# Optimization experiments

Hardware: AMD Instinct MI355X
Metric: run time of the kernel (lower is better)

The kernel has to match this reference:

```python
import jax, jax.numpy as jnp
import numpy as np

B, N, D = 2, 2048, 512
H, DH = 8, 64
P = 64  # position_max_embedding


def setup_inputs() -> dict:
    key = jax.random.key(0)
    ks = jax.random.split(key, 8)
    s = 0.02
    return {
        "x": jax.random.normal(ks[0], (B, N, D), jnp.float32),
        "Wq": jax.random.normal(ks[1], (D, H * DH), jnp.float32) * s,
        "Wk": jax.random.normal(ks[2], (D, H * DH), jnp.float32) * s,
        "Wv": jax.random.normal(ks[3], (D, H * DH), jnp.float32) * s,
        "rel_pos": jax.random.normal(ks[4], (2 * P + 1, H), jnp.float32) * s,
        "c_emb": jax.random.uniform(ks[5], (2 * P + 1, H), jnp.float32, 0.5, 1.5),
        "Wo": jax.random.normal(ks[6], (H * DH, D), jnp.float32) * s,
        "bo": jnp.zeros((D,), jnp.float32),
    }


def reference(x, Wq, Wk, Wv, rel_pos, c_emb, Wo, bo):
    b, n, _ = x.shape
    scale = DH ** -0.5
    q = (x @ Wq).reshape(b, n, H, DH)
    k = (x @ Wk).reshape(b, n, H, DH)
    v = (x @ Wv).reshape(b, n, H, DH)
    # relative position index: j - i, clamped to [-P, P], shifted to [0, 2P]
    idx = jnp.clip(jnp.arange(n)[None, :] - jnp.arange(n)[:, None], -P, P) + P  # [n, n]
    pos_bias = rel_pos[idx]          # [n, n, H]
    c_gate = c_emb[idx]              # [n, n, H]
    sim = jnp.einsum('bihd,bjhd->bhij', q, k)  # [b, H, n, n]
    sim = (sim + pos_bias.transpose(2, 0, 1)[None]) * scale
    attn = jax.nn.softmax(sim, axis=-1) * c_gate.transpose(2, 0, 1)[None]
    out = jnp.einsum('bhij,bjhd->bihd', attn, v).reshape(b, n, H * DH)
    return out @ Wo + bo
```

## Files before the change

kernel.cpp:

```cpp
#include <hip/hip_runtime.h>
#include <stdint.h>

#define BB 2
#define NN 2048
#define DD 512
#define HH 8
#define DHH 64

typedef __attribute__((ext_vector_type(8))) short bf16x8;
typedef __attribute__((ext_vector_type(4))) float f32x4;

#define LOG2E 1.44269504088896340736f

#if __has_builtin(__builtin_amdgcn_exp2f)
#define QSCALE (0.125f * LOG2E)
#define EXP2(x) __builtin_amdgcn_exp2f(x)
#else
#define QSCALE 0.125f
#define EXP2(x) __expf(x)
#endif

static __device__ __forceinline__ unsigned short f2bf(float f) {
    union { float f; unsigned u; } v; v.f = f;
    unsigned r = v.u + 0x7fffu + ((v.u >> 16) & 1u);
    return (unsigned short)(r >> 16);
}

static __device__ __forceinline__ unsigned pkbf(float a, float b) {
    union { float f; unsigned u; } ua, ub; ua.f = a; ub.f = b;
    return ((ub.u + 0x8000u) & 0xffff0000u) | ((ua.u + 0x8000u) >> 16);
}

static __device__ __forceinline__ bf16x8 ld8(const unsigned short* p) {
    bf16x8 v; __builtin_memcpy(&v, p, 16); return v;
}

static __device__ __forceinline__ void gld_lds16(const void* g, void* l) {
    __builtin_amdgcn_global_load_lds((const __attribute__((address_space(1))) void*)g,
                                     (__attribute__((address_space(3))) void*)l, 16, 0, 0);
}

__global__ void ca_prep(const float* __restrict__ x,
                        const float* __restrict__ w0, const float* __restrict__ w1,
                        const float* __restrict__ w2, const float* __restrict__ w3,
                        unsigned short* __restrict__ xb, unsigned short* __restrict__ wts) {
    __shared__ float T[64][65];
    int bx = blockIdx.x;
    if (bx < 2048) {
        int gid = bx * 256 + threadIdx.x;
        float4 v = ((const float4*)x)[gid];
        ushort4 o;
        o.x = f2bf(v.x); o.y = f2bf(v.y); o.z = f2bf(v.z); o.w = f2bf(v.w);
        ((ushort4*)xb)[gid] = o;
        return;
    }
    int bb = bx - 2048;
    int z = bb >> 6, t = bb & 63;
    const float* W = (z == 0) ? w0 : (z == 1) ? w1 : (z == 2) ? w2 : w3;
    unsigned short* out = wts + z * 262144;
    int k0 = (t & 7) << 6, n0 = (t >> 3) << 6;
    int c = threadIdx.x & 63, r4 = threadIdx.x >> 6;
#pragma unroll
    for (int rr = 0; rr < 16; ++rr) {
        int r = r4 * 16 + rr;
        T[r][c] = W[(k0 + r) * 512 + n0 + c];
    }
    __syncthreads();
#pragma unroll
    for (int rr = 0; rr < 16; ++rr) {
        int r = r4 * 16 + rr;
        out[(n0 + r) * 512 + k0 + c] = f2bf(T[c][r]);
    }
}

__global__ __launch_bounds__(256, 4)
void ca_gemm_proj(const unsigned short* __restrict__ A,
                  const unsigned short* __restrict__ wts,
                  unsigned short* __restrict__ qkv,
                  unsigned short* __restrict__ vt) {
    __shared__ __align__(16) unsigned short Ash[128 * 64];
    __shared__ __align__(16) unsigned short Bsh[64 * 64];
    int z = blockIdx.y >> 3;
    const unsigned short* BT = wts + z * 262144;
    unsigned short* out = qkv + z * 2097152;
    int w = threadIdx.x >> 6, lane = threadIdx.x & 63;
    int c = lane & 15, qd = lane >> 4;
    int m0 = blockIdx.x * 128 + w * 16;
    int n0 = (blockIdx.y & 7) * 64;

    int lr = lane >> 3, ls = lane & 7;
    int soff = lr * 512 + ((ls ^ (lr & 7)) << 3);
    const unsigned short* Ab = A + (blockIdx.x * 128) * 512 + soff;
    const unsigned short* Bb = BT + n0 * 512 + soff;

#pragma unroll
    for (int L = 0; L < 4; ++L)
        gld_lds16(Ab + (w * 32 + L * 8) * 512, (char*)Ash + (w * 32 + L * 8) * 128);
#pragma unroll
    for (int L = 0; L < 2; ++L)
        gld_lds16(Bb + (w * 16 + L * 8) * 512, (char*)Bsh + (w * 16 + L * 8) * 128);

    f32x4 acc[2][4];
#pragma unroll
    for (int mt = 0; mt < 2; ++mt)
#pragma unroll
        for (int nb = 0; nb < 4; ++nb) acc[mt][nb] = (f32x4){0.f, 0.f, 0.f, 0.f};

    int cs = c & 7;
    for (int k = 0; k < 8; ++k) {
        asm volatile("s_waitcnt vmcnt(0)" ::: "memory");
        __syncthreads();
        bf16x8 a[2][2], b[4][2];
#pragma unroll
        for (int mt = 0; mt < 2; ++mt)
#pragma unroll
            for (int kk = 0; kk < 2; ++kk)
                a[mt][kk] = ld8((const unsigned short*)((char*)Ash +
                                (w * 16 + mt * 64 + c) * 128 + (((kk * 4 + qd) ^ cs) << 4)));
#pragma unroll
        for (int nb = 0; nb < 4; ++nb)
#pragma unroll
            for (int kk = 0; kk < 2; ++kk)
                b[nb][kk] = ld8((const unsigned short*)((char*)Bsh +
                                (nb * 16 + c) * 128 + (((kk * 4 + qd) ^ cs) << 4)));
        asm volatile("s_waitcnt lgkmcnt(0)" ::: "memory");
        __syncthreads();
        if (k < 7) {
            int k0 = (k + 1) * 64;
#pragma unroll
            for (int L = 0; L < 4; ++L)
                gld_lds16(Ab + k0 + (w * 32 + L * 8) * 512, (char*)Ash + (w * 32 + L * 8) * 128);
#pragma unroll
            for (int L = 0; L < 2; ++L)
                gld_lds16(Bb + k0 + (w * 16 + L * 8) * 512, (char*)Bsh + (w * 16 + L * 8) * 128);
        }
#pragma unroll
        for (int kk = 0; kk < 2; ++kk)
#pragma unroll
            for (int nb = 0; nb < 4; ++nb) {
                acc[0][nb] = __builtin_amdgcn_mfma_f32_16x16x32_bf16(a[0][kk], b[nb][kk], acc[0][nb], 0, 0, 0);
                acc[1][nb] = __builtin_amdgcn_mfma_f32_16x16x32_bf16(a[1][kk], b[nb][kk], acc[1][nb], 0, 0, 0);
            }
    }

    if (z == 2) {
#pragma unroll
        for (int mt = 0; mt < 2; ++mt) {
            int ib = m0 + mt * 64 + qd * 4;
            int b = ib >> 11, i = ib & 2047;
#pragma unroll
            for (int nb = 0; nb < 4; ++nb) {
                int col = n0 + nb * 16 + c;
                int h = col >> 6, d = col & 63;
                ushort4 pk;
                pk.x = f2bf(acc[mt][nb][0]); pk.y = f2bf(acc[mt][nb][1]);
                pk.z = f2bf(acc[mt][nb][2]); pk.w = f2bf(acc[mt][nb][3]);
                *(ushort4*)(vt + (((b << 3) + h) * 64 + d) * 2048 + i) = pk;
            }
        }
    } else {
        float scale = (z == 0) ? QSCALE : 1.0f;
#pragma unroll
        for (int mt = 0; mt < 2; ++mt)
#pragma unroll
            for (int nb = 0; nb < 4; ++nb) {
#pragma unroll
                for (int r = 0; r < 4; ++r) {
                    int row = m0 + mt * 64 + qd * 4 + r;
                    int col = n0 + nb * 16 + c;
                    int b = row >> 11, i = row & 2047, h = col >> 6, d = col & 63;
                    out[(((b << 3) + h) * 2048 + i) * 64 + d] = f2bf(acc[mt][nb][r] * scale);
                }
            }
    }
}

__global__ __launch_bounds__(256, 4)
void ca_flash(const unsigned short* __restrict__ Q,
              const unsigned short* __restrict__ K,
              const unsigned short* __restrict__ VT,
              const float* __restrict__ rel_pos,
              const float* __restrict__ c_emb,
              unsigned short* __restrict__ Ob) {
    __shared__ __align__(16) char smem[37904];
    unsigned (*Ptu)[16][16] = (unsigned (*)[16][16])(smem + 32768);
    float* red = (float*)smem;
    float2* lrg = (float2*)(smem + 36864);

    int bx = blockIdx.x;
    int xcd = bx & 7, slot = bx >> 3;
    int bh = xcd + ((slot >> 6) << 3);
    int it = slot & 63;
    int b = bh >> 3, h = bh & 7;
    int w = threadIdx.x >> 6, lane = threadIdx.x & 63;
    int c = lane & 15, qd = lane >> 4;
    int i0 = it * 32;

    if (threadIdx.x < 129) {
        lrg[threadIdx.x] = make_float2(rel_pos[threadIdx.x * 8 + h] * QSCALE,
                                       c_emb[threadIdx.x * 8 + h]);
    }

    const unsigned short* Qh = Q  + bh * 131072;
    const unsigned short* Kh = K  + bh * 131072;
    const unsigned short* Vh = VT + bh * 131072;
    char* kw = smem + w * 4096;
    char* vw = smem + 16384 + w * 4096;

    int koff[4], voff[4];
#pragma unroll
    for (int L = 0; L < 4; ++L) {
        int kr = L * 8 + (lane >> 3);
        koff[L] = kr * 64 + (((lane & 7) ^ ((kr >> 1) & 7)) << 3);
        int vr = L * 16 + (lane >> 2);
        voff[L] = vr * 2048 + (((lane & 3) ^ ((lane >> 3) & 3)) << 3);
    }

    {
        int j0 = w * 32;
#pragma unroll
        for (int L = 0; L < 4; ++L) gld_lds16(Kh + j0 * 64 + koff[L], kw + L * 1024);
#pragma unroll
        for (int L = 0; L < 4; ++L) gld_lds16(Vh + j0 + voff[L], vw + L * 1024);
    }

    bf16x8 aq[2][2];
#pragma unroll
    for (int qt = 0; qt < 2; ++qt) {
        aq[qt][0] = ld8(Qh + (i0 + qt * 16 + c) * 64 + qd * 8);
        aq[qt][1] = ld8(Qh + (i0 + qt * 16 + c) * 64 + 32 + qd * 8);
    }

    f32x4 o2[2][4];
    float lp2[2][4];
#pragma unroll
    for (int qt = 0; qt < 2; ++qt)
#pragma unroll
        for (int db = 0; db < 4; ++db) {
            o2[qt][db] = (f32x4){0.f, 0.f, 0.f, 0.f};
            lp2[qt][db] = 0.f;
        }

    __syncthreads();

    int ksw  = c & 7;
    int vsw  = (c >> 1) & 3;

    for (int t = 0; t < 16; ++t) {
        asm volatile("s_waitcnt vmcnt(0)" ::: "memory");
        __builtin_amdgcn_sched_barrier(0);
        bf16x8 bk0a = ld8((const unsigned short*)(kw + (2 * c) * 128     + (((qd)     ^ ksw) << 4)));
        bf16x8 bk0b = ld8((const unsigned short*)(kw + (2 * c) * 128     + (((qd + 4) ^ ksw) << 4)));
        bf16x8 bk1a = ld8((const unsigned short*)(kw + (2 * c + 1) * 128 + (((qd)     ^ ksw) << 4)));
        bf16x8 bk1b = ld8((const unsigned short*)(kw + (2 * c + 1) * 128 + (((qd + 4) ^ ksw) << 4)));
        bf16x8 bv[4];
#pragma unroll
        for (int db = 0; db < 4; ++db)
            bv[db] = ld8((const unsigned short*)(vw + (db * 16 + c) * 64 + ((qd ^ vsw) << 4)));
        asm volatile("s_waitcnt lgkmcnt(0)" ::: "memory");
        __builtin_amdgcn_sched_barrier(0);
        if (t < 15) {
            int j0n = ((t + 1) * 4 + w) * 32;
#pragma unroll
            for (int L = 0; L < 4; ++L) gld_lds16(Kh + j0n * 64 + koff[L], kw + L * 1024);
#pragma unroll
            for (int L = 0; L < 4; ++L) gld_lds16(Vh + j0n + voff[L], vw + L * 1024);
        }

        int j0 = (t * 4 + w) * 32;
#pragma unroll
        for (int qt = 0; qt < 2; ++qt) {
            f32x4 s0 = (f32x4){0.f, 0.f, 0.f, 0.f};
            f32x4 s1 = (f32x4){0.f, 0.f, 0.f, 0.f};
            s0 = __builtin_amdgcn_mfma_f32_16x16x32_bf16(aq[qt][0], bk0a, s0, 0, 0, 0);
            s0 = __builtin_amdgcn_mfma_f32_16x16x32_bf16(aq[qt][1], bk0b, s0, 0, 0, 0);
            s1 = __builtin_amdgcn_mfma_f32_16x16x32_bf16(aq[qt][0], bk1a, s1, 0, 0, 0);
            s1 = __builtin_amdgcn_mfma_f32_16x16x32_bf16(aq[qt][1], bk1b, s1, 0, 0, 0);

            int iqt0 = i0 + qt * 16;
            int iq = iqt0 + qd * 4;
            bool lowc  = (j0 + 31 - iqt0) <= -64;
            bool highc = (j0 - (iqt0 + 15)) >= 64;
            if (lowc || highc) {
                int d = lowc ? 0 : 128;
                float2 gg = lrg[d];
#pragma unroll
                for (int r = 0; r < 4; ++r) {
                    float t0 = EXP2(s0[r] + gg.x);
                    float t1 = EXP2(s1[r] + gg.x);
                    lp2[qt][r] += t0 + t1;
                    Ptu[w][qd * 4 + r][c] = pkbf(t0 * gg.y, t1 * gg.y);
                }
            } else {
#pragma unroll
                for (int r = 0; r < 4; ++r) {
                    int i = iq + r;
                    int j = j0 + 2 * c;
                    int d0 = j - i;     d0 = (d0 < -64) ? -64 : (d0 > 64 ? 64 : d0); d0 += 64;
                    int d1 = j + 1 - i; d1 = (d1 < -64) ? -64 : (d1 > 64 ? 64 : d1); d1 += 64;
                    float2 g0 = lrg[d0];
                    float2 g1 = lrg[d1];
                    float t0 = EXP2(s0[r] + g0.x);
                    float t1 = EXP2(s1[r] + g1.x);
                    lp2[qt][r] += t0 + t1;
                    Ptu[w][qd * 4 + r][c] = pkbf(t0 * g0.y, t1 * g1.y);
                }
            }
            bf16x8 ap = ld8((const unsigned short*)&Ptu[w][c][0] + qd * 8);
#pragma unroll
            for (int db = 0; db < 4; ++db)
                o2[qt][db] = __builtin_amdgcn_mfma_f32_16x16x32_bf16(ap, bv[db], o2[qt][db], 0, 0, 0);
        }
    }

    __syncthreads();
    if (w > 0) {
        float* dst = red + (w - 1) * (64 * 41) + lane * 41;
#pragma unroll
        for (int qt = 0; qt < 2; ++qt)
#pragma unroll
            for (int db = 0; db < 4; ++db)
#pragma unroll
                for (int r = 0; r < 4; ++r)
                    dst[qt * 16 + db * 4 + r] = o2[qt][db][r];
#pragma unroll
        for (int qt = 0; qt < 2; ++qt)
#pragma unroll
            for (int r = 0; r < 4; ++r)
                dst[32 + qt * 4 + r] = lp2[qt][r];
    }
    __syncthreads();
    if (w == 0) {
#pragma unroll
        for (int ww = 0; ww < 3; ++ww) {
            const float* src = red + ww * (64 * 41) + lane * 41;
#pragma unroll
            for (int qt = 0; qt < 2; ++qt) {
#pragma unroll
                for (int db = 0; db < 4; ++db)
#pragma unroll
                    for (int r = 0; r < 4; ++r)
                        o2[qt][db][r] += src[qt * 16 + db * 4 + r];
#pragma unroll
                for (int r = 0; r < 4; ++r)
                    lp2[qt][r] += src[32 + qt * 4 + r];
            }
        }
#pragma unroll
        for (int qt = 0; qt < 2; ++qt)
#pragma unroll
            for (int r = 0; r < 4; ++r) {
                lp2[qt][r] += __shfl_xor(lp2[qt][r], 1);
                lp2[qt][r] += __shfl_xor(lp2[qt][r], 2);
                lp2[qt][r] += __shfl_xor(lp2[qt][r], 4);
                lp2[qt][r] += __shfl_xor(lp2[qt][r], 8);
            }
#pragma unroll
        for (int qt = 0; qt < 2; ++qt)
#pragma unroll
            for (int db = 0; db < 4; ++db)
#pragma unroll
                for (int r = 0; r < 4; ++r) {
                    int row = b * 2048 + i0 + qt * 16 + qd * 4 + r;
                    int col = h * 64 + db * 16 + c;
                    Ob[row * 512 + col] = f2bf(o2[qt][db][r] / lp2[qt][r]);
                }
    }
}

__global__ __launch_bounds__(256, 4)
void ca_gemm_out(const unsigned short* __restrict__ A,
                 const unsigned short* __restrict__ BT,
                 const float* __restrict__ bias,
                 float* __restrict__ out) {
    __shared__ __align__(16) unsigned short Ash[64 * 64];
    __shared__ __align__(16) unsigned short Bsh[64 * 64];
    int w = threadIdx.x >> 6, lane = threadIdx.x & 63;
    int c = lane & 15, qd = lane >> 4;
    int m0 = blockIdx.x * 64 + w * 16;
    int n0 = blockIdx.y * 64;

    int lr = lane >> 3, ls = lane & 7;
    int soff = lr * 512 + ((ls ^ (lr & 7)) << 3);
    const unsigned short* Ab = A + (blockIdx.x * 64) * 512 + soff;
    const unsigned short* Bb = BT + n0 * 512 + soff;

#pragma unroll
    for (int L = 0; L < 2; ++L) {
        gld_lds16(Ab + (w * 16 + L * 8) * 512, (char*)Ash + (w * 16 + L * 8) * 128);
        gld_lds16(Bb + (w * 16 + L * 8) * 512, (char*)Bsh + (w * 16 + L * 8) * 128);
    }

    f32x4 acc[4];
#pragma unroll
    for (int nb = 0; nb < 4; ++nb) acc[nb] = (f32x4){0.f, 0.f, 0.f, 0.f};

    int cs = c & 7;
    for (int k = 0; k < 8; ++k) {
        asm volatile("s_waitcnt vmcnt(0)" ::: "memory");
        __syncthreads();
        bf16x8 a[2], b[4][2];
#pragma unroll
        for (int kk = 0; kk < 2; ++kk)
            a[kk] = ld8((const unsigned short*)((char*)Ash +
                        (w * 16 + c) * 128 + (((kk * 4 + qd) ^ cs) << 4)));
#pragma unroll
        for (int nb = 0; nb < 4; ++nb)
#pragma unroll
            for (int kk = 0; kk < 2; ++kk)
                b[nb][kk] = ld8((const unsigned short*)((char*)Bsh +
                                (nb * 16 + c) * 128 + (((kk * 4 + qd) ^ cs) << 4)));
        asm volatile("s_waitcnt lgkmcnt(0)" ::: "memory");
        __syncthreads();
        if (k < 7) {
            int k0 = (k + 1) * 64;
#pragma unroll
            for (int L = 0; L < 2; ++L) {
                gld_lds16(Ab + k0 + (w * 16 + L * 8) * 512, (char*)Ash + (w * 16 + L * 8) * 128);
                gld_lds16(Bb + k0 + (w * 16 + L * 8) * 512, (char*)Bsh + (w * 16 + L * 8) * 128);
            }
        }
#pragma unroll
        for (int kk = 0; kk < 2; ++kk)
#pragma unroll
            for (int nb = 0; nb < 4; ++nb)
                acc[nb] = __builtin_amdgcn_mfma_f32_16x16x32_bf16(a[kk], b[nb][kk], acc[nb], 0, 0, 0);
    }
#pragma unroll
    for (int nb = 0; nb < 4; ++nb) {
#pragma unroll
        for (int r = 0; r < 4; ++r) {
            int row = m0 + qd * 4 + r;
            int col = n0 + nb * 16 + c;
            out[row * 512 + col] = acc[nb][r] + bias[col];
        }
    }
}

extern "C" void kernel_launch(void* const* d_in, const int* in_sizes, int n_in,
                              void* d_out, int out_size, void* d_ws, size_t ws_size,
                              hipStream_t stream) {
    const float* x   = (const float*)d_in[0];
    const float* Wq  = (const float*)d_in[1];
    const float* Wk  = (const float*)d_in[2];
    const float* Wv  = (const float*)d_in[3];
    const float* rel = (const float*)d_in[4];
    const float* cem = (const float*)d_in[5];
    const float* Wo  = (const float*)d_in[6];
    const float* bo  = (const float*)d_in[7];
    float* out = (float*)d_out;
    char* ws = (char*)d_ws;

    unsigned short* xb  = (unsigned short*)(ws);
    unsigned short* wts = (unsigned short*)(ws + 4194304);
    unsigned short* qkv = (unsigned short*)(ws + 6291456);
    unsigned short* vt  = (unsigned short*)(ws + 18874368);
    unsigned short* ob  = (unsigned short*)(ws + 23068672);

    hipLaunchKernelGGL(ca_prep, dim3(2304), dim3(256), 0, stream, x, Wq, Wk, Wv, Wo, xb, wts);
    hipLaunchKernelGGL(ca_gemm_proj, dim3(32, 24), dim3(256), 0, stream, xb, wts, qkv, vt);
    hipLaunchKernelGGL(ca_flash, dim3(1024), dim3(256), 0, stream,
                       qkv, qkv + 2097152, vt, rel, cem, ob);
    hipLaunchKernelGGL(ca_gemm_out, dim3(64, 8), dim3(256), 0, stream, ob, wts + 3 * 262144, bo, out);
}
```

Measured before the change: 142.4 us.

## Double-buffer LDS tiles in projection and output GEMMs to overlap loads

Both the QKV projection GEMM and the output GEMM now keep two LDS buffers. The next K-slice's global-to-LDS loads are issued before waiting on the current slice, using a partial vmcnt wait, and the loop is fully unrolled. This is meant to hide global load latency behind MFMA work instead of serializing load then compute. It doubles LDS use per block, and the projection kernel's occupancy hint drops from 4 to 3 blocks per CU.

```diff
diff --git a/kernel.cpp b/kernel.cpp
--- a/kernel.cpp
+++ b/kernel.cpp
@@ -73,13 +73,13 @@
     }
 }
 
-__global__ __launch_bounds__(256, 4)
+__global__ __launch_bounds__(256, 3)
 void ca_gemm_proj(const unsigned short* __restrict__ A,
                   const unsigned short* __restrict__ wts,
                   unsigned short* __restrict__ qkv,
                   unsigned short* __restrict__ vt) {
-    __shared__ __align__(16) unsigned short Ash[128 * 64];
-    __shared__ __align__(16) unsigned short Bsh[64 * 64];
+    __shared__ __align__(16) unsigned short Ash[2][128 * 64];
+    __shared__ __align__(16) unsigned short Bsh[2][64 * 64];
     int z = blockIdx.y >> 3;
     const unsigned short* BT = wts + z * 262144;
     unsigned short* out = qkv + z * 2097152;
@@ -95,10 +95,10 @@
 
 #pragma unroll
     for (int L = 0; L < 4; ++L)
-        gld_lds16(Ab + (w * 32 + L * 8) * 512, (char*)Ash + (w * 32 + L * 8) * 128);
+        gld_lds16(Ab + (w * 32 + L * 8) * 512, (char*)Ash[0] + (w * 32 + L * 8) * 128);
 #pragma unroll
     for (int L = 0; L < 2; ++L)
-        gld_lds16(Bb + (w * 16 + L * 8) * 512, (char*)Bsh + (w * 16 + L * 8) * 128);
+        gld_lds16(Bb + (w * 16 + L * 8) * 512, (char*)Bsh[0] + (w * 16 + L * 8) * 128);
 
     f32x4 acc[2][4];
 #pragma unroll
@@ -107,39 +107,43 @@
         for (int nb = 0; nb < 4; ++nb) acc[mt][nb] = (f32x4){0.f, 0.f, 0.f, 0.f};
 
     int cs = c & 7;
+#pragma unroll
     for (int k = 0; k < 8; ++k) {
-        asm volatile("s_waitcnt vmcnt(0)" ::: "memory");
+        int b = k & 1;
+        if (k < 7) {
+            int k0 = (k + 1) * 64;
+#pragma unroll
+            for (int L = 0; L < 4; ++L)
+                gld_lds16(Ab + k0 + (w * 32 + L * 8) * 512, (char*)Ash[b ^ 1] + (w * 32 + L * 8) * 128);
+#pragma unroll
+            for (int L = 0; L < 2; ++L)
+                gld_lds16(Bb + k0 + (w * 16 + L * 8) * 512, (char*)Bsh[b ^ 1] + (w * 16 + L * 8) * 128);
+            asm volatile("s_waitcnt vmcnt(6)" ::: "memory");
+        } else {
+            asm volatile("s_waitcnt vmcnt(0)" ::: "memory");
+        }
         __syncthreads();
-        bf16x8 a[2][2], b[4][2];
+        bf16x8 a[2][2], bq[4][2];
 #pragma unroll
         for (int mt = 0; mt < 2; ++mt)
 #pragma unroll
             for (int kk = 0; kk < 2; ++kk)
-                a[mt][kk] = ld8((const unsigned short*)((char*)Ash +
+                a[mt][kk] = ld8((const unsigned short*)((char*)Ash[b] +
                                 (w * 16 + mt * 64 + c) * 128 + (((kk * 4 + qd) ^ cs) << 4)));
 #pragma unroll
         for (int nb = 0; nb < 4; ++nb)
 #pragma unroll
             for (int kk = 0; kk < 2; ++kk)
-                b[nb][kk] = ld8((const unsigned short*)((char*)Bsh +
+                bq[nb][kk] = ld8((const unsigned short*)((char*)Bsh[b] +
                                 (nb * 16 + c) * 128 + (((kk * 4 + qd) ^ cs) << 4)));
         asm volatile("s_waitcnt lgkmcnt(0)" ::: "memory");
         __syncthreads();
-        if (k < 7) {
-            int k0 = (k + 1) * 64;
-#pragma unroll
-            for (int L = 0; L < 4; ++L)
-                gld_lds16(Ab + k0 + (w * 32 + L * 8) * 512, (char*)Ash + (w * 32 + L * 8) * 128);
-#pragma unroll
-            for (int L = 0; L < 2; ++L)
-                gld_lds16(Bb + k0 + (w * 16 + L * 8) * 512, (char*)Bsh + (w * 16 + L * 8) * 128);
-        }
 #pragma unroll
         for (int kk = 0; kk < 2; ++kk)
 #pragma unroll
             for (int nb = 0; nb < 4; ++nb) {
-                acc[0][nb] = __builtin_amdgcn_mfma_f32_16x16x32_bf16(a[0][kk], b[nb][kk], acc[0][nb], 0, 0, 0);
-                acc[1][nb] = __builtin_amdgcn_mfma_f32_16x16x32_bf16(a[1][kk], b[nb][kk], acc[1][nb], 0, 0, 0);
+                acc[0][nb] = __builtin_amdgcn_mfma_f32_16x16x32_bf16(a[0][kk], bq[nb][kk], acc[0][nb], 0, 0, 0);
+                acc[1][nb] = __builtin_amdgcn_mfma_f32_16x16x32_bf16(a[1][kk], bq[nb][kk], acc[1][nb], 0, 0, 0);
             }
     }
 
@@ -373,8 +377,8 @@
                  const unsigned short* __restrict__ BT,
                  const float* __restrict__ bias,
                  float* __restrict__ out) {
-    __shared__ __align__(16) unsigned short Ash[64 * 64];
-    __shared__ __align__(16) unsigned short Bsh[64 * 64];
+    __shared__ __align__(16) unsigned short Ash[2][64 * 64];
+    __shared__ __align__(16) unsigned short Bsh[2][64 * 64];
     int w = threadIdx.x >> 6, lane = threadIdx.x & 63;
     int c = lane & 15, qd = lane >> 4;
     int m0 = blockIdx.x * 64 + w * 16;
@@ -387,8 +391,8 @@
 
 #pragma unroll
     for (int L = 0; L < 2; ++L) {
-        gld_lds16(Ab + (w * 16 + L * 8) * 512, (char*)Ash + (w * 16 + L * 8) * 128);
-        gld_lds16(Bb + (w * 16 + L * 8) * 512, (char*)Bsh + (w * 16 + L * 8) * 128);
+        gld_lds16(Ab + (w * 16 + L * 8) * 512, (char*)Ash[0] + (w * 16 + L * 8) * 128);
+        gld_lds16(Bb + (w * 16 + L * 8) * 512, (char*)Bsh[0] + (w * 16 + L * 8) * 128);
     }
 
     f32x4 acc[4];
@@ -396,35 +400,39 @@
     for (int nb = 0; nb < 4; ++nb) acc[nb] = (f32x4){0.f, 0.f, 0.f, 0.f};
 
     int cs = c & 7;
+#pragma unroll
     for (int k = 0; k < 8; ++k) {
-        asm volatile("s_waitcnt vmcnt(0)" ::: "memory");
+        int b = k & 1;
+        if (k < 7) {
+            int k0 = (k + 1) * 64;
+#pragma unroll
+            for (int L = 0; L < 2; ++L) {
+                gld_lds16(Ab + k0 + (w * 16 + L * 8) * 512, (char*)Ash[b ^ 1] + (w * 16 + L * 8) * 128);
+                gld_lds16(Bb + k0 + (w * 16 + L * 8) * 512, (char*)Bsh[b ^ 1] + (w * 16 + L * 8) * 128);
+            }
+            asm volatile("s_waitcnt vmcnt(4)" ::: "memory");
+        } else {
+            asm volatile("s_waitcnt vmcnt(0)" ::: "memory");
+        }
         __syncthreads();
-        bf16x8 a[2], b[4][2];
+        bf16x8 a[2], bq[4][2];
 #pragma unroll
         for (int kk = 0; kk < 2; ++kk)
-            a[kk] = ld8((const unsigned short*)((char*)Ash +
+            a[kk] = ld8((const unsigned short*)((char*)Ash[b] +
                         (w * 16 + c) * 128 + (((kk * 4 + qd) ^ cs) << 4)));
 #pragma unroll
         for (int nb = 0; nb < 4; ++nb)
 #pragma unroll
             for (int kk = 0; kk < 2; ++kk)
-                b[nb][kk] = ld8((const unsigned short*)((char*)Bsh +
+                bq[nb][kk] = ld8((const unsigned short*)((char*)Bsh[b] +
                                 (nb * 16 + c) * 128 + (((kk * 4 + qd) ^ cs) << 4)));
         asm volatile("s_waitcnt lgkmcnt(0)" ::: "memory");
         __syncthreads();
-        if (k < 7) {
-            int k0 = (k + 1) * 64;
-#pragma unroll
-            for (int L = 0; L < 2; ++L) {
-                gld_lds16(Ab + k0 + (w * 16 + L * 8) * 512, (char*)Ash + (w * 16 + L * 8) * 128);
-                gld_lds16(Bb + k0 + (w * 16 + L * 8) * 512, (char*)Bsh + (w * 16 + L * 8) * 128);
-            }
-        }
 #pragma unroll
         for (int kk = 0; kk < 2; ++kk)
 #pragma unroll
             for (int nb = 0; nb < 4; ++nb)
-                acc[nb] = __builtin_amdgcn_mfma_f32_16x16x32_bf16(a[kk], b[nb][kk], acc[nb], 0, 0, 0);
+                acc[nb] = __builtin_amdgcn_mfma_f32_16x16x32_bf16(a[kk], bq[nb][kk], acc[nb], 0, 0, 0);
     }
 #pragma unroll
     for (int nb = 0; nb < 4; ++nb) {
```

Measured after the change: 139.2 us. 2.2% less time.
